# Kernel optimization log

Hardware: AMD Instinct MI355X
Metric: run time of the kernel (lower is better)

The kernel has to match this reference:

```python
import jax, jax.numpy as jnp
import numpy as np

N_NODES = 100000
N_EDGES = 1600000
DIM = 128
NUM_FEATURES = 128
NUM_LAYERS = 3


def _linear_params(key, fan_in, fan_out):
    kw, kb = jax.random.split(key)
    bound = 1.0 / np.sqrt(fan_in)
    W = jax.random.uniform(kw, (fan_in, fan_out), jnp.float32, -bound, bound)
    b = jax.random.uniform(kb, (fan_out,), jnp.float32, -bound, bound)
    return W, b


def setup_inputs() -> dict:
    key = jax.random.key(0)
    ks = jax.random.split(key, 16)
    x = jax.random.normal(ks[0], (N_NODES, NUM_FEATURES), jnp.float32)
    edge_index = jax.random.randint(ks[1], (2, N_EDGES), 0, N_NODES, jnp.int64)
    batch = jnp.zeros((N_NODES,), jnp.int64)
    inp = {"x": x, "edge_index": edge_index, "batch": batch}
    # GINConv MLPs: layer i has Linear(in, DIM) -> ReLU -> Linear(DIM, DIM)
    for i in range(NUM_LAYERS):
        fan_in = NUM_FEATURES if i == 0 else DIM
        W1, b1 = _linear_params(ks[2 + 2 * i], fan_in, DIM)
        W2, b2 = _linear_params(ks[3 + 2 * i], DIM, DIM)
        inp[f"W1_{i}"], inp[f"b1_{i}"] = W1, b1
        inp[f"W2_{i}"], inp[f"b2_{i}"] = W2, b2
    # readout == 'concat' -> final Linear(DIM * NUM_LAYERS, 1)
    Wm, bm = _linear_params(ks[10], DIM * NUM_LAYERS, 1)
    inp["Wm"], inp["bm"] = Wm, bm
    return inp


def _gin_layer(x, W1, b1, W2, b2, src, dst):
    # GINConv with eps=0: MLP(x_i + sum_{j->i} x_j)
    agg = jax.ops.segment_sum(x[src], dst, num_segments=N_NODES)  # [N, d]
    h = agg + x
    h = jnp.maximum(h @ W1 + b1, 0.0)
    return h @ W2 + b2


def _forward(x, params, Wm, bm, src, dst):
    xs = []
    for i in range(NUM_LAYERS):
        W1, b1, W2, b2 = params[i]
        x = _gin_layer(x, W1, b1, W2, b2, src, dst)
        if i != NUM_LAYERS - 1:
            x = jnp.maximum(x, 0.0)
        xs.append(x)
    node_prob = jnp.concatenate(xs, axis=1)  # readout == 'concat'
    return jax.nn.sigmoid(node_prob @ Wm + bm)


def reference(x, edge_index, batch,
              W1_0, b1_0, W2_0, b2_0,
              W1_1, b1_1, W2_1, b2_1,
              W1_2, b1_2, W2_2, b2_2,
              Wm, bm):
    src, dst = edge_index[0], edge_index[1]
    params = [(W1_0, b1_0, W2_0, b2_0),
              (W1_1, b1_1, W2_1, b2_1),
              (W1_2, b1_2, W2_2, b2_2)]
    return _forward(x, params, Wm, bm, src, dst)
```

## Files before the change

### kernel.cpp

```cpp
#include <hip/hip_runtime.h>
#include <hip/hip_bf16.h>

#define N_NODES 100000
#define N_EDGES 1600000
#define DIM 128

#define NB    782
#define NPB   128
#define BSTR  2944
#define CHUNK 4096

typedef __attribute__((ext_vector_type(8))) short bf16x8;
typedef __attribute__((ext_vector_type(4))) float f32x4;

__device__ __forceinline__ short f2bf(float f) {
    union { float f; unsigned u; } v; v.f = f;
    unsigned r = (v.u + 0x7fff + ((v.u >> 16) & 1)) >> 16;
    return (short)r;
}
__device__ __forceinline__ unsigned pk(float lo, float hi) {
    return (unsigned)(unsigned short)f2bf(lo) | ((unsigned)(unsigned short)f2bf(hi) << 16);
}
__device__ __forceinline__ float bl(unsigned p) {
    union { unsigned u; float f; } v; v.u = p << 16; return v.f;
}
__device__ __forceinline__ float bh(unsigned p) {
    union { unsigned u; float f; } v; v.u = p & 0xffff0000u; return v.f;
}
__device__ __forceinline__ float bfs(short s) {
    union { unsigned u; float f; } v; v.u = ((unsigned)(unsigned short)s) << 16; return v.f;
}

__global__ __launch_bounds__(256) void prep_kernel(
    const float* __restrict__ x, unsigned short* __restrict__ xb,
    const float* __restrict__ W0, const float* __restrict__ W1,
    const float* __restrict__ W2, const float* __restrict__ W3,
    const float* __restrict__ W4, const float* __restrict__ W5,
    unsigned short* __restrict__ T)
{
    int b = blockIdx.x, t = threadIdx.x;
    if (b < 6250) {
        long long i = (long long)b * 256 + t;
        const float4* p = (const float4*)(x + i * 8);
        float4 a = p[0], c = p[1];
        uint4 o;
        o.x = pk(a.x, a.y); o.y = pk(a.z, a.w);
        o.z = pk(c.x, c.y); o.w = pk(c.z, c.w);
        *(uint4*)(xb + i * 8) = o;
    } else {
        int idx = (b - 6250) * 256 + t;
        int m = idx >> 14, rem = idx & 16383;
        int n = rem >> 7, k = rem & 127;
        const float* W = (m == 0) ? W0 : (m == 1) ? W1 : (m == 2) ? W2
                       : (m == 3) ? W3 : (m == 4) ? W4 : W5;
        T[(size_t)m * DIM * DIM + n * DIM + k] = (unsigned short)f2bf(W[k * DIM + n]);
    }
}

__global__ __launch_bounds__(256) void bucketA_kernel(
    const int* __restrict__ src, const int* __restrict__ dst,
    int* __restrict__ gcur, unsigned* __restrict__ barr)
{
    __shared__ int cnt[NB];
    __shared__ int base[NB];
    const int t = threadIdx.x;
    const long long e0 = (long long)blockIdx.x * CHUNK;
    const int ecnt = (int)((e0 + CHUNK <= N_EDGES) ? CHUNK : (N_EDGES - e0));

    for (int i = t; i < NB; i += 256) cnt[i] = 0;
    __syncthreads();
    for (int i = t; i < ecnt; i += 256)
        atomicAdd(&cnt[dst[e0 + i] >> 7], 1);
    __syncthreads();
    for (int i = t; i < NB; i += 256) {
        int c = cnt[i];
        base[i] = c ? atomicAdd(&gcur[i], c) : 0;
        cnt[i] = 0;
    }
    __syncthreads();
    for (int i = t; i < ecnt; i += 256) {
        int d = dst[e0 + i], s = src[e0 + i];
        int bk = d >> 7;
        int r = atomicAdd(&cnt[bk], 1);
        barr[(long long)bk * BSTR + base[bk] + r] =
            (unsigned)s | ((unsigned)(d & 127) << 20);
    }
}

__global__ __launch_bounds__(64) void scanb_kernel(
    const int* __restrict__ gcur, int* __restrict__ cbase)
{
    int lane = threadIdx.x;
    int carry = 0;
    for (int b0 = 0; b0 < NB; b0 += 64) {
        int v = (b0 + lane < NB) ? gcur[b0 + lane] : 0;
        int s = v;
#pragma unroll
        for (int ofs = 1; ofs < 64; ofs <<= 1) {
            int u = __shfl_up(s, ofs);
            if (lane >= ofs) s += u;
        }
        if (b0 + lane < NB) cbase[b0 + lane] = carry + s - v;
        carry += __shfl(s, 63);
    }
    if (lane == 0) cbase[NB] = carry;
}

__global__ __launch_bounds__(256) void bucketB_kernel(
    const unsigned* __restrict__ barr, const int* __restrict__ gcur,
    const int* __restrict__ cbase, int* __restrict__ off, int* __restrict__ csr)
{
    __shared__ int cnt[NPB];
    __shared__ int cur[NPB];
    __shared__ int sbase, sn;
    const int b = blockIdx.x, t = threadIdx.x;
    if (t < NPB) cnt[t] = 0;
    if (t == 0) { sbase = cbase[b]; sn = gcur[b]; }
    __syncthreads();
    const int n = sn;
    const unsigned* be = barr + (long long)b * BSTR;
    for (int i = t; i < n; i += 256)
        atomicAdd(&cnt[(be[i] >> 20) & 127], 1);
    __syncthreads();
    if (t < 64) {
        int carry = 0;
#pragma unroll
        for (int k = 0; k < 2; ++k) {
            int idx = k * 64 + t;
            int v = cnt[idx], s = v;
#pragma unroll
            for (int ofs = 1; ofs < 64; ofs <<= 1) {
                int u = __shfl_up(s, ofs);
                if (t >= ofs) s += u;
            }
            cur[idx] = carry + s - v;
            carry += __shfl(s, 63);
        }
    }
    __syncthreads();
    if (t < NPB) {
        int node = b * NPB + t;
        if (node < N_NODES) off[node] = sbase + cur[t];
    }
    if (b == NB - 1 && t == 0) off[N_NODES] = cbase[NB];
    __syncthreads();
    for (int i = t; i < n; i += 256) {
        unsigned r = be[i];
        int j = (r >> 20) & 127;
        int p = atomicAdd(&cur[j], 1);
        csr[sbase + p] = (int)(r & 0xFFFFF);
    }
}

__global__ __launch_bounds__(256) void gather_kernel(
    const unsigned short* __restrict__ xb,
    const int* __restrict__ off, const int* __restrict__ csr,
    unsigned short* __restrict__ ab)
{
    long long gt = (long long)blockIdx.x * 256 + threadIdx.x;
    int node = (int)(gt >> 6);
    int lane = (int)(gt & 63);
    if (node >= N_NODES) return;
    const int g = lane >> 4, l4 = lane & 15;
    const int beg = off[node], end = off[node + 1];
    float acc[8] = {0.f, 0.f, 0.f, 0.f, 0.f, 0.f, 0.f, 0.f};
    int j = beg + g;
    for (; j + 12 < end; j += 16) {
        int s0 = csr[j], s1 = csr[j + 4], s2 = csr[j + 8], s3 = csr[j + 12];
        uint4 v0 = *(const uint4*)(xb + (long long)s0 * DIM + l4 * 8);
        uint4 v1 = *(const uint4*)(xb + (long long)s1 * DIM + l4 * 8);
        uint4 v2 = *(const uint4*)(xb + (long long)s2 * DIM + l4 * 8);
        uint4 v3 = *(const uint4*)(xb + (long long)s3 * DIM + l4 * 8);
        acc[0] += (bl(v0.x) + bl(v1.x)) + (bl(v2.x) + bl(v3.x));
        acc[1] += (bh(v0.x) + bh(v1.x)) + (bh(v2.x) + bh(v3.x));
        acc[2] += (bl(v0.y) + bl(v1.y)) + (bl(v2.y) + bl(v3.y));
        acc[3] += (bh(v0.y) + bh(v1.y)) + (bh(v2.y) + bh(v3.y));
        acc[4] += (bl(v0.z) + bl(v1.z)) + (bl(v2.z) + bl(v3.z));
        acc[5] += (bh(v0.z) + bh(v1.z)) + (bh(v2.z) + bh(v3.z));
        acc[6] += (bl(v0.w) + bl(v1.w)) + (bl(v2.w) + bl(v3.w));
        acc[7] += (bh(v0.w) + bh(v1.w)) + (bh(v2.w) + bh(v3.w));
    }
    for (; j < end; j += 4) {
        int s = csr[j];
        uint4 v = *(const uint4*)(xb + (long long)s * DIM + l4 * 8);
        acc[0] += bl(v.x); acc[1] += bh(v.x);
        acc[2] += bl(v.y); acc[3] += bh(v.y);
        acc[4] += bl(v.z); acc[5] += bh(v.z);
        acc[6] += bl(v.w); acc[7] += bh(v.w);
    }
#pragma unroll
    for (int k = 0; k < 8; ++k) {
        acc[k] += __shfl_xor(acc[k], 16);
        acc[k] += __shfl_xor(acc[k], 32);
    }
    if (g == 0) {
        uint4 sv = *(const uint4*)(xb + (long long)node * DIM + l4 * 8);
        acc[0] += bl(sv.x); acc[1] += bh(sv.x);
        acc[2] += bl(sv.y); acc[3] += bh(sv.y);
        acc[4] += bl(sv.z); acc[5] += bh(sv.z);
        acc[6] += bl(sv.w); acc[7] += bh(sv.w);
        uint4 o;
        o.x = pk(acc[0], acc[1]); o.y = pk(acc[2], acc[3]);
        o.z = pk(acc[4], acc[5]); o.w = pk(acc[6], acc[7]);
        *(uint4*)(ab + (long long)node * DIM + l4 * 8) = o;
    }
}

__global__ __launch_bounds__(256) void gin_mlp_kernel(
    const unsigned short* __restrict__ ab,
    const unsigned short* __restrict__ Wt1, const float* __restrict__ b1,
    const unsigned short* __restrict__ Wt2, const float* __restrict__ b2,
    unsigned short* __restrict__ outb,
    const unsigned short* __restrict__ hb0, const unsigned short* __restrict__ hb1,
    const float* __restrict__ Wm, const float* __restrict__ bm,
    float* __restrict__ out, int mode, int N)
{
    __shared__ short S[128][136];

    const int t = threadIdx.x;
    const long long row0 = (long long)blockIdx.x * 128;
    const int r = t >> 1, half = t & 1, c0 = half * 64;
    const long long gr = row0 + r;

    if (gr < N) {
        const unsigned short* pa = ab + gr * DIM + c0;
#pragma unroll
        for (int v = 0; v < 8; ++v)
            *(uint4*)&S[r][c0 + v * 8] = *(const uint4*)(pa + v * 8);
    } else {
#pragma unroll
        for (int v = 0; v < 8; ++v)
            *(uint4*)&S[r][c0 + v * 8] = make_uint4(0, 0, 0, 0);
    }
    __syncthreads();

    const int w = t >> 6, lane = t & 63;
    const int wr = (w >> 1) * 64, wc = (w & 1) * 64;
    const int fr = lane & 15, kg = lane >> 4;

    f32x4 acc[4][4] = {};
#pragma unroll
    for (int k0 = 0; k0 < 128; k0 += 32) {
        bf16x8 a[4], b[4];
#pragma unroll
        for (int mi = 0; mi < 4; ++mi)
            a[mi] = *(const bf16x8*)&S[wr + mi * 16 + fr][k0 + kg * 8];
#pragma unroll
        for (int ni = 0; ni < 4; ++ni)
            b[ni] = *(const bf16x8*)(Wt1 + (long long)(wc + ni * 16 + fr) * DIM + k0 + kg * 8);
#pragma unroll
        for (int mi = 0; mi < 4; ++mi)
#pragma unroll
            for (int ni = 0; ni < 4; ++ni)
                acc[mi][ni] = __builtin_amdgcn_mfma_f32_16x16x32_bf16(
                    a[mi], b[ni], acc[mi][ni], 0, 0, 0);
    }
    __syncthreads();

    {
        float bia[4];
#pragma unroll
        for (int ni = 0; ni < 4; ++ni) bia[ni] = b1[wc + ni * 16 + fr];
#pragma unroll
        for (int mi = 0; mi < 4; ++mi)
#pragma unroll
            for (int ni = 0; ni < 4; ++ni)
#pragma unroll
                for (int j = 0; j < 4; ++j) {
                    int rr = wr + mi * 16 + kg * 4 + j;
                    int cc = wc + ni * 16 + fr;
                    float hv = acc[mi][ni][j] + bia[ni];
                    S[rr][cc] = f2bf(hv > 0.f ? hv : 0.f);
                }
    }
    __syncthreads();

    f32x4 acc2[4][4] = {};
#pragma unroll
    for (int k0 = 0; k0 < 128; k0 += 32) {
        bf16x8 a[4], b[4];
#pragma unroll
        for (int mi = 0; mi < 4; ++mi)
            a[mi] = *(const bf16x8*)&S[wr + mi * 16 + fr][k0 + kg * 8];
#pragma unroll
        for (int ni = 0; ni < 4; ++ni)
            b[ni] = *(const bf16x8*)(Wt2 + (long long)(wc + ni * 16 + fr) * DIM + k0 + kg * 8);
#pragma unroll
        for (int mi = 0; mi < 4; ++mi)
#pragma unroll
            for (int ni = 0; ni < 4; ++ni)
                acc2[mi][ni] = __builtin_amdgcn_mfma_f32_16x16x32_bf16(
                    a[mi], b[ni], acc2[mi][ni], 0, 0, 0);
    }
    __syncthreads();

    {
        float bia[4];
#pragma unroll
        for (int ni = 0; ni < 4; ++ni) bia[ni] = b2[wc + ni * 16 + fr];
#pragma unroll
        for (int mi = 0; mi < 4; ++mi)
#pragma unroll
            for (int ni = 0; ni < 4; ++ni)
#pragma unroll
                for (int j = 0; j < 4; ++j) {
                    int rr = wr + mi * 16 + kg * 4 + j;
                    int cc = wc + ni * 16 + fr;
                    float v2 = acc2[mi][ni][j] + bia[ni];
                    if (mode == 1 && v2 < 0.f) v2 = 0.f;
                    S[rr][cc] = f2bf(v2);
                }
    }
    __syncthreads();

    if (mode == 1) {
        if (gr < N) {
            unsigned short* po = outb + gr * DIM + c0;
#pragma unroll
            for (int v = 0; v < 8; ++v)
                *(uint4*)(po + v * 8) = *(const uint4*)&S[r][c0 + v * 8];
        }
    } else {
        float s = 0.f;
        if (gr < N) {
            const unsigned short* p0 = hb0 + gr * DIM + c0;
            const unsigned short* p1 = hb1 + gr * DIM + c0;
#pragma unroll
            for (int v = 0; v < 8; ++v) {
                uint4 u0 = *(const uint4*)(p0 + v * 8);
                uint4 u1 = *(const uint4*)(p1 + v * 8);
                const float* wm0 = Wm + c0 + v * 8;
                const float* wm1 = Wm + 128 + c0 + v * 8;
                s += bl(u0.x) * wm0[0] + bh(u0.x) * wm0[1]
                   + bl(u0.y) * wm0[2] + bh(u0.y) * wm0[3]
                   + bl(u0.z) * wm0[4] + bh(u0.z) * wm0[5]
                   + bl(u0.w) * wm0[6] + bh(u0.w) * wm0[7];
                s += bl(u1.x) * wm1[0] + bh(u1.x) * wm1[1]
                   + bl(u1.y) * wm1[2] + bh(u1.y) * wm1[3]
                   + bl(u1.z) * wm1[4] + bh(u1.z) * wm1[5]
                   + bl(u1.w) * wm1[6] + bh(u1.w) * wm1[7];
            }
            const float* wm2 = Wm + 256 + c0;
#pragma unroll
            for (int c = 0; c < 64; ++c)
                s += bfs(S[r][c0 + c]) * wm2[c];
        }
        s += __shfl_xor(s, 1);
        if (half == 0 && gr < N)
            out[gr] = 1.f / (1.f + __expf(-(s + bm[0])));
    }
}

extern "C" void kernel_launch(void* const* d_in, const int* in_sizes, int n_in,
                              void* d_out, int out_size, void* d_ws, size_t ws_size,
                              hipStream_t stream)
{
    const float* x  = (const float*)d_in[0];
    const int*   ei = (const int*)d_in[1];
    const int*   src = ei;
    const int*   dst = ei + N_EDGES;
    const float* W1[3] = { (const float*)d_in[3], (const float*)d_in[7],  (const float*)d_in[11] };
    const float* b1[3] = { (const float*)d_in[4], (const float*)d_in[8],  (const float*)d_in[12] };
    const float* W2[3] = { (const float*)d_in[5], (const float*)d_in[9],  (const float*)d_in[13] };
    const float* b2[3] = { (const float*)d_in[6], (const float*)d_in[10], (const float*)d_in[14] };
    const float* Wm = (const float*)d_in[15];
    const float* bm = (const float*)d_in[16];
    float* out = (float*)d_out;

    char* p = (char*)d_ws;
    unsigned short* xb = (unsigned short*)p; p += (size_t)N_NODES * DIM * 2;
    unsigned short* ab = (unsigned short*)p; p += (size_t)N_NODES * DIM * 2;
    unsigned short* hb = (unsigned short*)p; p += (size_t)2 * N_NODES * DIM * 2;
    unsigned short* Wt = (unsigned short*)p; p += (size_t)6 * DIM * DIM * 2;
    int* off  = (int*)p;     p += (size_t)(N_NODES + 1) * sizeof(int);
    int* csr  = (int*)p;     p += (size_t)N_EDGES * sizeof(int);
    int* gcur = (int*)p;     p += (size_t)NB * sizeof(int);
    int* cbase = (int*)p;    p += (size_t)(NB + 1) * sizeof(int);
    unsigned* barr = (unsigned*)p; p += (size_t)NB * BSTR * sizeof(unsigned);

    const int mlp_blocks  = (N_NODES + 127) / 128;
    const int wave_blocks = (N_NODES * 64 + 255) / 256;
    const int pa_blocks   = (N_EDGES + CHUNK - 1) / CHUNK;

    hipMemsetAsync(gcur, 0, (size_t)NB * sizeof(int), stream);
    bucketA_kernel<<<pa_blocks, 256, 0, stream>>>(src, dst, gcur, barr);
    scanb_kernel<<<1, 64, 0, stream>>>(gcur, cbase);
    bucketB_kernel<<<NB, 256, 0, stream>>>(barr, gcur, cbase, off, csr);

    prep_kernel<<<6250 + 384, 256, 0, stream>>>(
        x, xb, W1[0], W2[0], W1[1], W2[1], W1[2], W2[2], Wt);

    unsigned short* hbuf[2] = { hb, hb + (size_t)N_NODES * DIM };
    const unsigned short* xin_b = xb;
    for (int layer = 0; layer < 3; ++layer) {
        gather_kernel<<<wave_blocks, 256, 0, stream>>>(xin_b, off, csr, ab);
        int mode = (layer != 2) ? 1 : 2;
        gin_mlp_kernel<<<mlp_blocks, 256, 0, stream>>>(
            ab, Wt + (size_t)(2 * layer) * DIM * DIM, b1[layer],
            Wt + (size_t)(2 * layer + 1) * DIM * DIM, b2[layer],
            (mode == 1) ? hbuf[layer] : (unsigned short*)nullptr,
            hbuf[0], hbuf[1], Wm, bm, out, mode, N_NODES);
        if (mode == 1) xin_b = hbuf[layer];
    }
}
```

Before: 478.7 us.

## Fuse neighbor aggregation into GIN MLP kernel via shared memory

Merges the per-node gather/sum kernel into the MLP kernel: each wave aggregates 32 nodes' neighbor features directly into the LDS tile, then MFMA MLP runs on it. This removes the global write and re-read of the aggregated buffer and one launch per layer. In exchange, gather parallelism drops sharply (782 blocks, sequential per-wave node loop), reducing memory-level parallelism for random gathers and serializing gather before MLP within each block.

```diff
diff --git a/kernel.cpp b/kernel.cpp
--- a/kernel.cpp
+++ b/kernel.cpp
@@ -152,62 +152,9 @@
     }
 }
 
-__global__ __launch_bounds__(256) void gather_kernel(
+__global__ __launch_bounds__(256, 3) void gin_fused_kernel(
     const unsigned short* __restrict__ xb,
     const int* __restrict__ off, const int* __restrict__ csr,
-    unsigned short* __restrict__ ab)
-{
-    long long gt = (long long)blockIdx.x * 256 + threadIdx.x;
-    int node = (int)(gt >> 6);
-    int lane = (int)(gt & 63);
-    if (node >= N_NODES) return;
-    const int g = lane >> 4, l4 = lane & 15;
-    const int beg = off[node], end = off[node + 1];
-    float acc[8] = {0.f, 0.f, 0.f, 0.f, 0.f, 0.f, 0.f, 0.f};
-    int j = beg + g;
-    for (; j + 12 < end; j += 16) {
-        int s0 = csr[j], s1 = csr[j + 4], s2 = csr[j + 8], s3 = csr[j + 12];
-        uint4 v0 = *(const uint4*)(xb + (long long)s0 * DIM + l4 * 8);
-        uint4 v1 = *(const uint4*)(xb + (long long)s1 * DIM + l4 * 8);
-        uint4 v2 = *(const uint4*)(xb + (long long)s2 * DIM + l4 * 8);
-        uint4 v3 = *(const uint4*)(xb + (long long)s3 * DIM + l4 * 8);
-        acc[0] += (bl(v0.x) + bl(v1.x)) + (bl(v2.x) + bl(v3.x));
-        acc[1] += (bh(v0.x) + bh(v1.x)) + (bh(v2.x) + bh(v3.x));
-        acc[2] += (bl(v0.y) + bl(v1.y)) + (bl(v2.y) + bl(v3.y));
-        acc[3] += (bh(v0.y) + bh(v1.y)) + (bh(v2.y) + bh(v3.y));
-        acc[4] += (bl(v0.z) + bl(v1.z)) + (bl(v2.z) + bl(v3.z));
-        acc[5] += (bh(v0.z) + bh(v1.z)) + (bh(v2.z) + bh(v3.z));
-        acc[6] += (bl(v0.w) + bl(v1.w)) + (bl(v2.w) + bl(v3.w));
-        acc[7] += (bh(v0.w) + bh(v1.w)) + (bh(v2.w) + bh(v3.w));
-    }
-    for (; j < end; j += 4) {
-        int s = csr[j];
-        uint4 v = *(const uint4*)(xb + (long long)s * DIM + l4 * 8);
-        acc[0] += bl(v.x); acc[1] += bh(v.x);
-        acc[2] += bl(v.y); acc[3] += bh(v.y);
-        acc[4] += bl(v.z); acc[5] += bh(v.z);
-        acc[6] += bl(v.w); acc[7] += bh(v.w);
-    }
-#pragma unroll
-    for (int k = 0; k < 8; ++k) {
-        acc[k] += __shfl_xor(acc[k], 16);
-        acc[k] += __shfl_xor(acc[k], 32);
-    }
-    if (g == 0) {
-        uint4 sv = *(const uint4*)(xb + (long long)node * DIM + l4 * 8);
-        acc[0] += bl(sv.x); acc[1] += bh(sv.x);
-        acc[2] += bl(sv.y); acc[3] += bh(sv.y);
-        acc[4] += bl(sv.z); acc[5] += bh(sv.z);
-        acc[6] += bl(sv.w); acc[7] += bh(sv.w);
-        uint4 o;
-        o.x = pk(acc[0], acc[1]); o.y = pk(acc[2], acc[3]);
-        o.z = pk(acc[4], acc[5]); o.w = pk(acc[6], acc[7]);
-        *(uint4*)(ab + (long long)node * DIM + l4 * 8) = o;
-    }
-}
-
-__global__ __launch_bounds__(256) void gin_mlp_kernel(
-    const unsigned short* __restrict__ ab,
     const unsigned short* __restrict__ Wt1, const float* __restrict__ b1,
     const unsigned short* __restrict__ Wt2, const float* __restrict__ b2,
     unsigned short* __restrict__ outb,
@@ -218,23 +165,64 @@
     __shared__ short S[128][136];
 
     const int t = threadIdx.x;
+    const int w = t >> 6, lane = t & 63;
     const long long row0 = (long long)blockIdx.x * 128;
-    const int r = t >> 1, half = t & 1, c0 = half * 64;
-    const long long gr = row0 + r;
-
-    if (gr < N) {
-        const unsigned short* pa = ab + gr * DIM + c0;
-#pragma unroll
-        for (int v = 0; v < 8; ++v)
-            *(uint4*)&S[r][c0 + v * 8] = *(const uint4*)(pa + v * 8);
-    } else {
-#pragma unroll
-        for (int v = 0; v < 8; ++v)
-            *(uint4*)&S[r][c0 + v * 8] = make_uint4(0, 0, 0, 0);
-    }
-    __syncthreads();
-
-    const int w = t >> 6, lane = t & 63;
+
+    {
+        const int g = lane >> 4, l4 = lane & 15;
+        for (int i = 0; i < 32; ++i) {
+            const int r = w * 32 + i;
+            const long long node = row0 + r;
+            float acc[8] = {0.f, 0.f, 0.f, 0.f, 0.f, 0.f, 0.f, 0.f};
+            if (node < N) {
+                const int beg = off[node], end = off[node + 1];
+                int j = beg + g;
+                for (; j + 12 < end; j += 16) {
+                    int s0 = csr[j], s1 = csr[j + 4], s2 = csr[j + 8], s3 = csr[j + 12];
+                    uint4 v0 = *(const uint4*)(xb + (long long)s0 * DIM + l4 * 8);
+                    uint4 v1 = *(const uint4*)(xb + (long long)s1 * DIM + l4 * 8);
+                    uint4 v2 = *(const uint4*)(xb + (long long)s2 * DIM + l4 * 8);
+                    uint4 v3 = *(const uint4*)(xb + (long long)s3 * DIM + l4 * 8);
+                    acc[0] += (bl(v0.x) + bl(v1.x)) + (bl(v2.x) + bl(v3.x));
+                    acc[1] += (bh(v0.x) + bh(v1.x)) + (bh(v2.x) + bh(v3.x));
+                    acc[2] += (bl(v0.y) + bl(v1.y)) + (bl(v2.y) + bl(v3.y));
+                    acc[3] += (bh(v0.y) + bh(v1.y)) + (bh(v2.y) + bh(v3.y));
+                    acc[4] += (bl(v0.z) + bl(v1.z)) + (bl(v2.z) + bl(v3.z));
+                    acc[5] += (bh(v0.z) + bh(v1.z)) + (bh(v2.z) + bh(v3.z));
+                    acc[6] += (bl(v0.w) + bl(v1.w)) + (bl(v2.w) + bl(v3.w));
+                    acc[7] += (bh(v0.w) + bh(v1.w)) + (bh(v2.w) + bh(v3.w));
+                }
+                for (; j < end; j += 4) {
+                    int s = csr[j];
+                    uint4 v = *(const uint4*)(xb + (long long)s * DIM + l4 * 8);
+                    acc[0] += bl(v.x); acc[1] += bh(v.x);
+                    acc[2] += bl(v.y); acc[3] += bh(v.y);
+                    acc[4] += bl(v.z); acc[5] += bh(v.z);
+                    acc[6] += bl(v.w); acc[7] += bh(v.w);
+                }
+            }
+#pragma unroll
+            for (int k = 0; k < 8; ++k) {
+                acc[k] += __shfl_xor(acc[k], 16);
+                acc[k] += __shfl_xor(acc[k], 32);
+            }
+            if (g == 0) {
+                if (node < N) {
+                    uint4 sv = *(const uint4*)(xb + node * DIM + l4 * 8);
+                    acc[0] += bl(sv.x); acc[1] += bh(sv.x);
+                    acc[2] += bl(sv.y); acc[3] += bh(sv.y);
+                    acc[4] += bl(sv.z); acc[5] += bh(sv.z);
+                    acc[6] += bl(sv.w); acc[7] += bh(sv.w);
+                }
+                uint4 o;
+                o.x = pk(acc[0], acc[1]); o.y = pk(acc[2], acc[3]);
+                o.z = pk(acc[4], acc[5]); o.w = pk(acc[6], acc[7]);
+                *(uint4*)&S[r][l4 * 8] = o;
+            }
+        }
+    }
+    __syncthreads();
+
     const int wr = (w >> 1) * 64, wc = (w & 1) * 64;
     const int fr = lane & 15, kg = lane >> 4;
 
@@ -313,6 +301,8 @@
     }
     __syncthreads();
 
+    const int r = t >> 1, half = t & 1, c0 = half * 64;
+    const long long gr = row0 + r;
     if (mode == 1) {
         if (gr < N) {
             unsigned short* po = outb + gr * DIM + c0;
@@ -369,7 +359,6 @@
 
     char* p = (char*)d_ws;
     unsigned short* xb = (unsigned short*)p; p += (size_t)N_NODES * DIM * 2;
-    unsigned short* ab = (unsigned short*)p; p += (size_t)N_NODES * DIM * 2;
     unsigned short* hb = (unsigned short*)p; p += (size_t)2 * N_NODES * DIM * 2;
     unsigned short* Wt = (unsigned short*)p; p += (size_t)6 * DIM * DIM * 2;
     int* off  = (int*)p;     p += (size_t)(N_NODES + 1) * sizeof(int);
@@ -379,7 +368,6 @@
     unsigned* barr = (unsigned*)p; p += (size_t)NB * BSTR * sizeof(unsigned);
 
     const int mlp_blocks  = (N_NODES + 127) / 128;
-    const int wave_blocks = (N_NODES * 64 + 255) / 256;
     const int pa_blocks   = (N_EDGES + CHUNK - 1) / CHUNK;
 
     hipMemsetAsync(gcur, 0, (size_t)NB * sizeof(int), stream);
@@ -393,10 +381,10 @@
     unsigned short* hbuf[2] = { hb, hb + (size_t)N_NODES * DIM };
     const unsigned short* xin_b = xb;
     for (int layer = 0; layer < 3; ++layer) {
-        gather_kernel<<<wave_blocks, 256, 0, stream>>>(xin_b, off, csr, ab);
         int mode = (layer != 2) ? 1 : 2;
-        gin_mlp_kernel<<<mlp_blocks, 256, 0, stream>>>(
-            ab, Wt + (size_t)(2 * layer) * DIM * DIM, b1[layer],
+        gin_fused_kernel<<<mlp_blocks, 256, 0, stream>>>(
+            xin_b, off, csr,
+            Wt + (size_t)(2 * layer) * DIM * DIM, b1[layer],
             Wt + (size_t)(2 * layer + 1) * DIM * DIM, b2[layer],
             (mode == 1) ? hbuf[layer] : (unsigned short*)nullptr,
             hbuf[0], hbuf[1], Wm, bm, out, mode, N_NODES);
```

Result: slower. 791.2 us (+65.3%).

## Fuse bucketing with prep kernel and drop global scan via padded CSR ranges

Applied to the files above, without the earlier changes.

The edge-bucketing pass is merged into the bf16 conversion/weight-transpose kernel as extra blocks, so one launch covers both. The single-block scan kernel is removed: the CSR is laid out with a fixed stride per bucket, and each node stores its own (begin, end) pair instead of a global prefix offset. This removes two launches and a serial one-wave scan, at the cost of a larger, sparser CSR buffer and an 8-byte range load per node in the gather kernel.

```diff
diff --git a/kernel.cpp b/kernel.cpp
--- a/kernel.cpp
+++ b/kernel.cpp
@@ -9,6 +9,7 @@
 #define NPB   128
 #define BSTR  2944
 #define CHUNK 4096
+#define PA_BLOCKS 391
 
 typedef __attribute__((ext_vector_type(8))) short bf16x8;
 typedef __attribute__((ext_vector_type(4))) float f32x4;
@@ -31,16 +32,42 @@
     union { unsigned u; float f; } v; v.u = ((unsigned)(unsigned short)s) << 16; return v.f;
 }
 
-__global__ __launch_bounds__(256) void prep_kernel(
+__global__ __launch_bounds__(256) void prepA_kernel(
+    const int* __restrict__ src, const int* __restrict__ dst,
+    int* __restrict__ gcur, unsigned* __restrict__ barr,
     const float* __restrict__ x, unsigned short* __restrict__ xb,
     const float* __restrict__ W0, const float* __restrict__ W1,
     const float* __restrict__ W2, const float* __restrict__ W3,
     const float* __restrict__ W4, const float* __restrict__ W5,
     unsigned short* __restrict__ T)
 {
-    int b = blockIdx.x, t = threadIdx.x;
-    if (b < 6250) {
-        long long i = (long long)b * 256 + t;
+    __shared__ int cnt[NB];
+    __shared__ int base[NB];
+    const int b = blockIdx.x, t = threadIdx.x;
+
+    if (b < PA_BLOCKS) {
+        const long long e0 = (long long)b * CHUNK;
+        const int ecnt = (int)((e0 + CHUNK <= N_EDGES) ? CHUNK : (N_EDGES - e0));
+        for (int i = t; i < NB; i += 256) cnt[i] = 0;
+        __syncthreads();
+        for (int i = t; i < ecnt; i += 256)
+            atomicAdd(&cnt[dst[e0 + i] >> 7], 1);
+        __syncthreads();
+        for (int i = t; i < NB; i += 256) {
+            int c = cnt[i];
+            base[i] = c ? atomicAdd(&gcur[i], c) : 0;
+            cnt[i] = 0;
+        }
+        __syncthreads();
+        for (int i = t; i < ecnt; i += 256) {
+            int d = dst[e0 + i], s = src[e0 + i];
+            int bk = d >> 7;
+            int r = atomicAdd(&cnt[bk], 1);
+            barr[(long long)bk * BSTR + base[bk] + r] =
+                (unsigned)s | ((unsigned)(d & 127) << 20);
+        }
+    } else if (b < PA_BLOCKS + 6250) {
+        long long i = (long long)(b - PA_BLOCKS) * 256 + t;
         const float4* p = (const float4*)(x + i * 8);
         float4 a = p[0], c = p[1];
         uint4 o;
@@ -48,7 +75,7 @@
         o.z = pk(c.x, c.y); o.w = pk(c.z, c.w);
         *(uint4*)(xb + i * 8) = o;
     } else {
-        int idx = (b - 6250) * 256 + t;
+        int idx = (b - PA_BLOCKS - 6250) * 256 + t;
         int m = idx >> 14, rem = idx & 16383;
         int n = rem >> 7, k = rem & 127;
         const float* W = (m == 0) ? W0 : (m == 1) ? W1 : (m == 2) ? W2
@@ -57,65 +84,17 @@
     }
 }
 
-__global__ __launch_bounds__(256) void bucketA_kernel(
-    const int* __restrict__ src, const int* __restrict__ dst,
-    int* __restrict__ gcur, unsigned* __restrict__ barr)
-{
-    __shared__ int cnt[NB];
-    __shared__ int base[NB];
-    const int t = threadIdx.x;
-    const long long e0 = (long long)blockIdx.x * CHUNK;
-    const int ecnt = (int)((e0 + CHUNK <= N_EDGES) ? CHUNK : (N_EDGES - e0));
-
-    for (int i = t; i < NB; i += 256) cnt[i] = 0;
-    __syncthreads();
-    for (int i = t; i < ecnt; i += 256)
-        atomicAdd(&cnt[dst[e0 + i] >> 7], 1);
-    __syncthreads();
-    for (int i = t; i < NB; i += 256) {
-        int c = cnt[i];
-        base[i] = c ? atomicAdd(&gcur[i], c) : 0;
-        cnt[i] = 0;
-    }
-    __syncthreads();
-    for (int i = t; i < ecnt; i += 256) {
-        int d = dst[e0 + i], s = src[e0 + i];
-        int bk = d >> 7;
-        int r = atomicAdd(&cnt[bk], 1);
-        barr[(long long)bk * BSTR + base[bk] + r] =
-            (unsigned)s | ((unsigned)(d & 127) << 20);
-    }
-}
-
-__global__ __launch_bounds__(64) void scanb_kernel(
-    const int* __restrict__ gcur, int* __restrict__ cbase)
-{
-    int lane = threadIdx.x;
-    int carry = 0;
-    for (int b0 = 0; b0 < NB; b0 += 64) {
-        int v = (b0 + lane < NB) ? gcur[b0 + lane] : 0;
-        int s = v;
-#pragma unroll
-        for (int ofs = 1; ofs < 64; ofs <<= 1) {
-            int u = __shfl_up(s, ofs);
-            if (lane >= ofs) s += u;
-        }
-        if (b0 + lane < NB) cbase[b0 + lane] = carry + s - v;
-        carry += __shfl(s, 63);
-    }
-    if (lane == 0) cbase[NB] = carry;
-}
-
 __global__ __launch_bounds__(256) void bucketB_kernel(
     const unsigned* __restrict__ barr, const int* __restrict__ gcur,
-    const int* __restrict__ cbase, int* __restrict__ off, int* __restrict__ csr)
+    int2* __restrict__ rng, int* __restrict__ csr)
 {
     __shared__ int cnt[NPB];
     __shared__ int cur[NPB];
-    __shared__ int sbase, sn;
+    __shared__ int sn;
     const int b = blockIdx.x, t = threadIdx.x;
+    const int sbase = b * BSTR;
     if (t < NPB) cnt[t] = 0;
-    if (t == 0) { sbase = cbase[b]; sn = gcur[b]; }
+    if (t == 0) sn = gcur[b];
     __syncthreads();
     const int n = sn;
     const unsigned* be = barr + (long long)b * BSTR;
@@ -140,9 +119,11 @@
     __syncthreads();
     if (t < NPB) {
         int node = b * NPB + t;
-        if (node < N_NODES) off[node] = sbase + cur[t];
-    }
-    if (b == NB - 1 && t == 0) off[N_NODES] = cbase[NB];
+        if (node < N_NODES) {
+            int beg = sbase + cur[t];
+            rng[node] = make_int2(beg, beg + cnt[t]);
+        }
+    }
     __syncthreads();
     for (int i = t; i < n; i += 256) {
         unsigned r = be[i];
@@ -154,7 +135,7 @@
 
 __global__ __launch_bounds__(256) void gather_kernel(
     const unsigned short* __restrict__ xb,
-    const int* __restrict__ off, const int* __restrict__ csr,
+    const int2* __restrict__ rng, const int* __restrict__ csr,
     unsigned short* __restrict__ ab)
 {
     long long gt = (long long)blockIdx.x * 256 + threadIdx.x;
@@ -162,7 +143,8 @@
     int lane = (int)(gt & 63);
     if (node >= N_NODES) return;
     const int g = lane >> 4, l4 = lane & 15;
-    const int beg = off[node], end = off[node + 1];
+    const int2 be = rng[node];
+    const int beg = be.x, end = be.y;
     float acc[8] = {0.f, 0.f, 0.f, 0.f, 0.f, 0.f, 0.f, 0.f};
     int j = beg + g;
     for (; j + 12 < end; j += 16) {
@@ -372,28 +354,25 @@
     unsigned short* ab = (unsigned short*)p; p += (size_t)N_NODES * DIM * 2;
     unsigned short* hb = (unsigned short*)p; p += (size_t)2 * N_NODES * DIM * 2;
     unsigned short* Wt = (unsigned short*)p; p += (size_t)6 * DIM * DIM * 2;
-    int* off  = (int*)p;     p += (size_t)(N_NODES + 1) * sizeof(int);
-    int* csr  = (int*)p;     p += (size_t)N_EDGES * sizeof(int);
+    int2* rng = (int2*)p;    p += (size_t)N_NODES * sizeof(int2);
+    int* csr  = (int*)p;     p += (size_t)NB * BSTR * sizeof(int);
     int* gcur = (int*)p;     p += (size_t)NB * sizeof(int);
-    int* cbase = (int*)p;    p += (size_t)(NB + 1) * sizeof(int);
     unsigned* barr = (unsigned*)p; p += (size_t)NB * BSTR * sizeof(unsigned);
 
     const int mlp_blocks  = (N_NODES + 127) / 128;
     const int wave_blocks = (N_NODES * 64 + 255) / 256;
-    const int pa_blocks   = (N_EDGES + CHUNK - 1) / CHUNK;
+    const int prepA_blocks = PA_BLOCKS + 6250 + 384;
 
     hipMemsetAsync(gcur, 0, (size_t)NB * sizeof(int), stream);
-    bucketA_kernel<<<pa_blocks, 256, 0, stream>>>(src, dst, gcur, barr);
-    scanb_kernel<<<1, 64, 0, stream>>>(gcur, cbase);
-    bucketB_kernel<<<NB, 256, 0, stream>>>(barr, gcur, cbase, off, csr);
-
-    prep_kernel<<<6250 + 384, 256, 0, stream>>>(
-        x, xb, W1[0], W2[0], W1[1], W2[1], W1[2], W2[2], Wt);
+    prepA_kernel<<<prepA_blocks, 256, 0, stream>>>(
+        src, dst, gcur, barr, x, xb,
+        W1[0], W2[0], W1[1], W2[1], W1[2], W2[2], Wt);
+    bucketB_kernel<<<NB, 256, 0, stream>>>(barr, gcur, rng, csr);
 
     unsigned short* hbuf[2] = { hb, hb + (size_t)N_NODES * DIM };
     const unsigned short* xin_b = xb;
     for (int layer = 0; layer < 3; ++layer) {
-        gather_kernel<<<wave_blocks, 256, 0, stream>>>(xin_b, off, csr, ab);
+        gather_kernel<<<wave_blocks, 256, 0, stream>>>(xin_b, rng, csr, ab);
         int mode = (layer != 2) ? 1 : 2;
         gin_mlp_kernel<<<mlp_blocks, 256, 0, stream>>>(
             ab, Wt + (size_t)(2 * layer) * DIM * DIM, b1[layer],
```

Result: faster. 468.3 us (-2.2%).
